# Performance work log

Hardware: AMD Instinct MI355X
Metric: run time of the kernel (lower is better)

Reference implementation:

```python
import jax, jax.numpy as jnp
import numpy as np

N = 50000   # nodes
IN = 256    # in_feats
OUT = 256   # out_feats
R = 4       # num relations
E = 80000   # edges per relation


def setup_inputs() -> dict:
    key = jax.random.key(0)
    ks = jax.random.split(key, 5)
    x = jax.random.normal(ks[0], (N, IN), jnp.float32)
    src = jax.random.randint(ks[1], (R, E), 0, N, jnp.int32)
    dst = jax.random.randint(ks[2], (R, E), 0, N, jnp.int32)
    # xavier_uniform with relu gain sqrt(2)
    limit = np.sqrt(2.0) * np.sqrt(6.0 / (IN + OUT))
    weight = jax.random.uniform(ks[3], (R, IN, OUT), jnp.float32, -limit, limit)
    self_loop_weight = jax.random.uniform(ks[4], (IN, OUT), jnp.float32, -limit, limit)
    bias = jnp.zeros((OUT,), jnp.float32)
    return dict(x=x, src=src, dst=dst, weight=weight,
                self_loop_weight=self_loop_weight, bias=bias)


def reference(x, src, dst, weight, self_loop_weight, bias):
    n = x.shape[0]

    def per_rel(s, d, W):
        # GraphConv(norm='right', weight=W): sum incoming messages, divide by
        # in-degree (clamped to 1), then matmul (in_feats == out_feats path).
        agg = jax.ops.segment_sum(x[s], d, num_segments=n)            # [N, IN]
        deg = jax.ops.segment_sum(jnp.ones(d.shape, x.dtype), d, num_segments=n)
        agg = agg / jnp.maximum(deg, 1.0)[:, None]
        return agg @ W                                                # [N, OUT]

    # HeteroGraphConv default aggregation: sum over relations
    msg = jax.vmap(per_rel)(src, dst, weight).sum(axis=0)             # [N, OUT]
    out = msg + x @ self_loop_weight + bias
    return jax.nn.relu(out)
```

## Files before the change

### kernel.cpp

```cpp
#include <hip/hip_runtime.h>

#define NODES 50000
#define FEAT  256
#define RELS  4
#define EDGES 80000
#define NEDGE (RELS * EDGES)
#define NB    (RELS * NODES)
#define NBSC  196
#define KSTEPS 40
#define CHUNKEL ((size_t)NODES * FEAT)

typedef __bf16 bf16x8  __attribute__((ext_vector_type(8)));
typedef float  floatx4 __attribute__((ext_vector_type(4)));

struct BF8U { union { unsigned short u[8]; bf16x8 v; uint4 q; }; };

static __device__ __forceinline__ unsigned short f2bf(float f) {
  union { float f; unsigned u; } v; v.f = f;
  unsigned r = v.u + 0x7FFFu + ((v.u >> 16) & 1u);
  return (unsigned short)(r >> 16);
}
static __device__ __forceinline__ bf16x8 cvt8(const float* p, float s) {
  float4 a = ((const float4*)p)[0], b = ((const float4*)p)[1];
  BF8U r;
  r.u[0] = f2bf(a.x * s); r.u[1] = f2bf(a.y * s);
  r.u[2] = f2bf(a.z * s); r.u[3] = f2bf(a.w * s);
  r.u[4] = f2bf(b.x * s); r.u[5] = f2bf(b.y * s);
  r.u[6] = f2bf(b.z * s); r.u[7] = f2bf(b.w * s);
  return r.v;
}

__global__ __launch_bounds__(256) void zero_kernel(unsigned* __restrict__ cnt) {
  int i = blockIdx.x * 256 + threadIdx.x;
  if (i < NB) cnt[i] = 0u;
}

__global__ __launch_bounds__(256) void count_kernel(const int* __restrict__ dst,
                                                    unsigned* __restrict__ cnt) {
  int e = blockIdx.x * 256 + threadIdx.x;
  if (e < NEDGE) atomicAdd(&cnt[(e / EDGES) * NODES + dst[e]], 1u);
}

__global__ __launch_bounds__(256) void scan1_kernel(const unsigned* __restrict__ cnt,
                                                    unsigned* __restrict__ bsum) {
  __shared__ unsigned red[4];
  int t = threadIdx.x;
  int i = blockIdx.x * 1024 + t * 4;
  unsigned s = 0;
  if (i + 3 < NB) {
    uint4 v = *(const uint4*)(cnt + i);
    s = v.x + v.y + v.z + v.w;
  } else {
    for (int j = 0; j < 4; ++j) if (i + j < NB) s += cnt[i + j];
  }
  for (int o = 32; o > 0; o >>= 1) s += __shfl_down(s, o);
  if ((t & 63) == 0) red[t >> 6] = s;
  __syncthreads();
  if (t == 0) bsum[blockIdx.x] = red[0] + red[1] + red[2] + red[3];
}

__global__ __launch_bounds__(256) void scan2_kernel(unsigned* __restrict__ bsum) {
  __shared__ unsigned sa[256], sb[256];
  int t = threadIdx.x;
  unsigned v = (t < NBSC) ? bsum[t] : 0u;
  sa[t] = v;
  __syncthreads();
  unsigned* pin = sa; unsigned* pout = sb;
  for (int d = 1; d < 256; d <<= 1) {
    pout[t] = pin[t] + ((t >= d) ? pin[t - d] : 0u);
    __syncthreads();
    unsigned* tmp = pin; pin = pout; pout = tmp;
  }
  if (t < NBSC) bsum[t] = pin[t] - v;
}

__global__ __launch_bounds__(256) void scan3_kernel(const unsigned* __restrict__ cnt,
                                                    const unsigned* __restrict__ bsum,
                                                    unsigned* __restrict__ off,
                                                    unsigned* __restrict__ cur) {
  __shared__ unsigned sa[256], sb[256];
  int t = threadIdx.x;
  int i = blockIdx.x * 1024 + t * 4;
  uint4 v = {0u, 0u, 0u, 0u};
  if (i + 3 < NB) {
    v = *(const uint4*)(cnt + i);
  } else {
    unsigned tmp[4] = {0u, 0u, 0u, 0u};
    for (int j = 0; j < 4; ++j) if (i + j < NB) tmp[j] = cnt[i + j];
    v.x = tmp[0]; v.y = tmp[1]; v.z = tmp[2]; v.w = tmp[3];
  }
  unsigned s = v.x + v.y + v.z + v.w;
  sa[t] = s;
  __syncthreads();
  unsigned* pin = sa; unsigned* pout = sb;
  for (int d = 1; d < 256; d <<= 1) {
    pout[t] = pin[t] + ((t >= d) ? pin[t - d] : 0u);
    __syncthreads();
    unsigned* tmp = pin; pin = pout; pout = tmp;
  }
  unsigned base = bsum[blockIdx.x] + pin[t] - s;
  uint4 o;
  o.x = base; o.y = o.x + v.x; o.z = o.y + v.y; o.w = o.z + v.z;
  if (i + 3 < NB) {
    *(uint4*)(off + i) = o;
    *(uint4*)(cur + i) = o;
  } else {
    unsigned oo[4] = {o.x, o.y, o.z, o.w};
    for (int j = 0; j < 4; ++j) if (i + j < NB) { off[i + j] = oo[j]; cur[i + j] = oo[j]; }
  }
  if (blockIdx.x == 0 && t == 0) off[NB] = NEDGE;
}

__global__ __launch_bounds__(256) void fill_kernel(const int* __restrict__ src,
                                                   const int* __restrict__ dst,
                                                   unsigned* __restrict__ cur,
                                                   unsigned* __restrict__ epk) {
  int e = blockIdx.x * 256 + threadIdx.x;
  if (e < NEDGE) {
    int r = e / EDGES;
    unsigned pos = atomicAdd(&cur[r * NODES + dst[e]], 1u);
    epk[pos] = (unsigned)src[e];
  }
}

__global__ __launch_bounds__(256) void prepack_kernel(const float* __restrict__ w,
                                                      const float* __restrict__ sw,
                                                      unsigned short* __restrict__ bpk) {
  int t = blockIdx.x * 256 + threadIdx.x;
  int ln = t & 63, nc = (t >> 6) & 15, kc = t >> 10;
  int col = nc * 16 + (ln & 15);
  int row0 = kc * 32 + (ln >> 4) * 8;
  BF8U vv;
#pragma unroll
  for (int j = 0; j < 8; ++j) {
    int gk = row0 + j;
    int c = gk >> 8, kr = gk & 255;
    const float* sp = (c < 4) ? (w + (size_t)c * 65536) : sw;
    vv.u[j] = f2bf(sp[(size_t)kr * 256 + col]);
  }
  ((uint4*)bpk)[t] = vv.q;
}

__global__ __launch_bounds__(256) void gather_kernel(
    const float* __restrict__ x, const unsigned* __restrict__ off,
    const unsigned* __restrict__ epk, unsigned short* __restrict__ agg) {
  int b = blockIdx.x * 4 + (threadIdx.x >> 6);
  int lane = threadIdx.x & 63;
  if (b >= NB) return;
  unsigned lo = off[b], hi = off[b + 1];
  float4 acc = {0.f, 0.f, 0.f, 0.f};
  unsigned e = lo;
  for (; e + 2 <= hi; e += 2) {
    int s0 = (int)epk[e], s1 = (int)epk[e + 1];
    float4 v0 = *(const float4*)(x + (size_t)s0 * FEAT + lane * 4);
    float4 v1 = *(const float4*)(x + (size_t)s1 * FEAT + lane * 4);
    acc.x += v0.x + v1.x; acc.y += v0.y + v1.y;
    acc.z += v0.z + v1.z; acc.w += v0.w + v1.w;
  }
  if (e < hi) {
    int s = (int)epk[e];
    float4 v = *(const float4*)(x + (size_t)s * FEAT + lane * 4);
    acc.x += v.x; acc.y += v.y; acc.z += v.z; acc.w += v.w;
  }
  unsigned dg = hi - lo;
  float sc = 1.0f / (float)(dg ? dg : 1u);
  unsigned short o[4] = { f2bf(acc.x * sc), f2bf(acc.y * sc),
                          f2bf(acc.z * sc), f2bf(acc.w * sc) };
  *(uint2*)(agg + (size_t)b * FEAT + lane * 4) = *(const uint2*)o;
}

__global__ __launch_bounds__(256, 3) void gemm_kernel(
    const unsigned short* __restrict__ agg, const float* __restrict__ x,
    const unsigned short* __restrict__ bpk, const float* __restrict__ bias,
    float* __restrict__ out) {
  __shared__ uint4 sA[4][256];
  const int tid = threadIdx.x;
  const int lane = tid & 63, wave = tid >> 6;
  const int quad = lane >> 4, l15 = lane & 15;
  const int m0 = blockIdx.x * 64;
  const int nbase = wave * 4;

  const int sl = tid & 3;
  const int trow = tid >> 2;
  int row_g = m0 + trow; if (row_g >= NODES) row_g = NODES - 1;
  const int widx = trow * 4 + (sl ^ ((trow >> 1) & 3));
  const int pswz = quad ^ ((l15 >> 1) & 3);

  const uint4* aggu4 = (const uint4*)agg;

  auto loadA = [&](int t) -> uint4 {
    if (t < 32) {
      return aggu4[(size_t)(t >> 3) * (CHUNKEL / 8) + (size_t)row_g * 32 +
                   (size_t)((t & 7) * 4 + sl)];
    } else {
      BF8U r;
      r.v = cvt8(x + (size_t)row_g * 256 + (t & 7) * 32 + sl * 8, 1.0f);
      return r.q;
    }
  };

#define SYNC_TILE()                                                            \
  do {                                                                         \
    asm volatile("s_waitcnt lgkmcnt(0)" ::: "memory");                         \
    __builtin_amdgcn_sched_barrier(0);                                         \
    __builtin_amdgcn_s_barrier();                                              \
    __builtin_amdgcn_sched_barrier(0);                                         \
  } while (0)

#define READ_A(bidx, dst)                                                      \
  { _Pragma("unroll") for (int ms = 0; ms < 4; ++ms)                           \
      dst[ms].q = sA[bidx][(ms * 16 + l15) * 4 + pswz]; }

#define LOAD_B(kc, dst)                                                        \
  {                                                                            \
    _Pragma("unroll") for (int ns = 0; ns < 4; ++ns) {                         \
      BF8U t_; t_.q = bp4[(size_t)(kc) * 1024 + (nbase + ns) * 64 + lane];     \
      dst[ns] = t_.v;                                                          \
    }                                                                          \
  }
#define MFMA16(af, bf)                                                         \
  _Pragma("unroll") for (int ms = 0; ms < 4; ++ms)                             \
    _Pragma("unroll") for (int ns = 0; ns < 4; ++ns)                           \
      acc[ms][ns] = __builtin_amdgcn_mfma_f32_16x16x32_bf16(af[ms].v, bf[ns],  \
                                                            acc[ms][ns], 0, 0, 0);

  floatx4 acc[4][4] = {};
  const uint4* bp4 = (const uint4*)bpk;
  bf16x8 b0[4], b1[4];
  BF8U a[4];

  uint4 rP = loadA(0);
  uint4 rO = loadA(1);
  uint4 rE = loadA(2);
  sA[0][widx] = rP;
  LOAD_B(0, b0);
  SYNC_TILE();

  for (int kc = 0; kc < KSTEPS; kc += 2) {
    READ_A(kc & 3, a);
    sA[(kc + 1) & 3][widx] = rO;
    if (kc + 3 < KSTEPS) rO = loadA(kc + 3);
    LOAD_B(kc + 1, b1);
    MFMA16(a, b0);
    SYNC_TILE();

    READ_A((kc + 1) & 3, a);
    if (kc + 2 < KSTEPS) {
      sA[(kc + 2) & 3][widx] = rE;
      LOAD_B(kc + 2, b0);
    }
    if (kc + 4 < KSTEPS) rE = loadA(kc + 4);
    MFMA16(a, b1);
    SYNC_TILE();
  }
#undef SYNC_TILE
#undef READ_A
#undef LOAD_B
#undef MFMA16

#pragma unroll
  for (int ms = 0; ms < 4; ++ms)
#pragma unroll
    for (int i = 0; i < 4; ++i) {
      int row = m0 + ms * 16 + quad * 4 + i;
      if (row < NODES) {
        float* op = out + (size_t)row * FEAT + wave * 64;
#pragma unroll
        for (int ns = 0; ns < 4; ++ns) {
          int col = ns * 16 + l15;
          op[col] = fmaxf(acc[ms][ns][i] + bias[wave * 64 + col], 0.0f);
        }
      }
    }
}

#define AROWS 128
#define ASTR  260
#define ABLK  512

__global__ __launch_bounds__(ABLK) void rgcn_fallback(
    const float* __restrict__ x, const int* __restrict__ src,
    const int* __restrict__ dst, const float* __restrict__ w,
    const float* __restrict__ sw, const float* __restrict__ bias,
    float* __restrict__ out) {
  __shared__ float sAgg[AROWS * ASTR];
  __shared__ unsigned short sB[8192];
  __shared__ unsigned sDeg[AROWS];
  const int tid = threadIdx.x, wave = tid >> 6, lane = tid & 63;
  const int quad = lane >> 4, l15 = lane & 15;
  const int m0 = blockIdx.x * AROWS;
  const int wrow = wave * 16;
  floatx4 acc[16] = {};
  const floatx4 fz = {0.f, 0.f, 0.f, 0.f};
  for (int r = 0; r < RELS; ++r) {
    for (int t = tid; t < (AROWS * ASTR) / 4; t += ABLK) ((floatx4*)sAgg)[t] = fz;
    if (tid < AROWS) sDeg[tid] = 0u;
    __syncthreads();
    const int4* sr4 = (const int4*)(src + r * EDGES);
    const int4* dr4 = (const int4*)(dst + r * EDGES);
    for (int i0 = tid; i0 < 20480; i0 += ABLK) {
      int4 d4 = {-1, -1, -1, -1}, s4 = {0, 0, 0, 0};
      if (i0 < EDGES / 4) { d4 = dr4[i0]; s4 = sr4[i0]; }
      int dd[4] = {d4.x, d4.y, d4.z, d4.w};
      int ss[4] = {s4.x, s4.y, s4.z, s4.w};
#pragma unroll
      for (int j = 0; j < 4; ++j) {
        unsigned u = (unsigned)(dd[j] - m0);
        unsigned long long mb = __ballot(u < (unsigned)AROWS);
        while (mb) {
          int jl = (int)__ffsll(mb) - 1; mb &= mb - 1;
          int s = __shfl(ss[j], jl);
          int ul = __shfl((int)u, jl);
          if (lane == 0) atomicAdd(&sDeg[ul], 1u);
          const float* xp = x + (size_t)s * FEAT + lane;
          float* ap = sAgg + ul * ASTR + lane;
#pragma unroll
          for (int k = 0; k < 4; ++k) atomicAdd(ap + k * 64, xp[k * 64]);
        }
      }
    }
    __syncthreads();
    unsigned dg = sDeg[wrow + l15];
    float rs = 1.0f / (float)(dg ? dg : 1u);
    const float* Wc = w + (size_t)r * 65536;
    for (int kc = 0; kc < 8; ++kc) {
      for (int t = tid; t < 1024; t += ABLK) {
        int ln = t & 63, nc = t >> 6;
        const float* wp = Wc + (size_t)(kc * 32 + (ln >> 4) * 8) * 256 + nc * 16 + (ln & 15);
        BF8U vv;
#pragma unroll
        for (int j = 0; j < 8; ++j) vv.u[j] = f2bf(wp[(size_t)j * 256]);
        ((uint4*)sB)[t] = vv.q;
      }
      __syncthreads();
      bf16x8 a = cvt8(&sAgg[(wrow + l15) * ASTR + kc * 32 + quad * 8], rs);
#pragma unroll
      for (int ns = 0; ns < 16; ++ns) {
        BF8U b8; b8.q = ((const uint4*)sB)[ns * 64 + lane];
        acc[ns] = __builtin_amdgcn_mfma_f32_16x16x32_bf16(a, b8.v, acc[ns], 0, 0, 0);
      }
      __syncthreads();
    }
  }
  {
    int row = m0 + wrow + l15;
    if (row >= NODES) row = NODES - 1;
    for (int kc = 0; kc < 8; ++kc) {
      for (int t = tid; t < 1024; t += ABLK) {
        int ln = t & 63, nc = t >> 6;
        const float* wp = sw + (size_t)(kc * 32 + (ln >> 4) * 8) * 256 + nc * 16 + (ln & 15);
        BF8U vv;
#pragma unroll
        for (int j = 0; j < 8; ++j) vv.u[j] = f2bf(wp[(size_t)j * 256]);
        ((uint4*)sB)[t] = vv.q;
      }
      __syncthreads();
      bf16x8 a = cvt8(x + (size_t)row * FEAT + kc * 32 + quad * 8, 1.0f);
#pragma unroll
      for (int ns = 0; ns < 16; ++ns) {
        BF8U b8; b8.q = ((const uint4*)sB)[ns * 64 + lane];
        acc[ns] = __builtin_amdgcn_mfma_f32_16x16x32_bf16(a, b8.v, acc[ns], 0, 0, 0);
      }
      __syncthreads();
    }
  }
#pragma unroll
  for (int i = 0; i < 4; ++i) {
    int row = m0 + wrow + quad * 4 + i;
    if (row < NODES) {
      float* op = out + (size_t)row * FEAT;
#pragma unroll
      for (int ns = 0; ns < 16; ++ns) {
        int col = ns * 16 + l15;
        op[col] = fmaxf(acc[ns][i] + bias[col], 0.0f);
      }
    }
  }
}

extern "C" void kernel_launch(void* const* d_in, const int* in_sizes, int n_in,
                              void* d_out, int out_size, void* d_ws, size_t ws_size,
                              hipStream_t stream) {
  const float* x    = (const float*)d_in[0];
  const int*   src  = (const int*)d_in[1];
  const int*   dst  = (const int*)d_in[2];
  const float* w    = (const float*)d_in[3];
  const float* sw   = (const float*)d_in[4];
  const float* bias = (const float*)d_in[5];
  float*       out  = (float*)d_out;
  char* ws = (char*)d_ws;

  const size_t NEED = 106736400;
  if (ws_size >= NEED) {
    unsigned short* bpk = (unsigned short*)ws;
    unsigned* cnt  = (unsigned*)(ws + 655360);
    unsigned* off  = (unsigned*)(ws + 1455360);
    unsigned* cur  = (unsigned*)(ws + 2255376);
    unsigned* epk  = (unsigned*)(ws + 3055376);
    unsigned* bsum = (unsigned*)(ws + 4335376);
    unsigned short* agg = (unsigned short*)(ws + 4336400);

    zero_kernel<<<(NB + 255) / 256, 256, 0, stream>>>(cnt);
    count_kernel<<<(NEDGE + 255) / 256, 256, 0, stream>>>(dst, cnt);
    scan1_kernel<<<NBSC, 256, 0, stream>>>(cnt, bsum);
    scan2_kernel<<<1, 256, 0, stream>>>(bsum);
    scan3_kernel<<<NBSC, 256, 0, stream>>>(cnt, bsum, off, cur);
    fill_kernel<<<(NEDGE + 255) / 256, 256, 0, stream>>>(src, dst, cur, epk);
    prepack_kernel<<<160, 256, 0, stream>>>(w, sw, bpk);
    gather_kernel<<<(NB + 3) / 4, 256, 0, stream>>>(x, off, epk, agg);
    gemm_kernel<<<(NODES + 63) / 64, 256, 0, stream>>>(agg, x, bpk, bias, out);
  } else {
    rgcn_fallback<<<391, ABLK, 0, stream>>>(x, src, dst, w, sw, bias, out);
  }
}
```

Before: 259.6 us.

## Fuse CSR build, prepack and gather into one persistent kernel with grid barriers

Replaces eight separate launches (zero, count, three scan stages, fill, prepack, gather) with one persistent kernel of 1536 blocks that separates the phases with atomic-counter grid barriers, plus a memset of the barrier counter. The aim is to remove per-launch overhead and the idle gaps between the small setup kernels. The gather loop is also unrolled to four edges per iteration to put more loads in flight. The grid barrier assumes all 1536 blocks are co-resident (8 per CU is requested via launch bounds), and it risks deadlock or spin overhead if they are not.

```diff
diff --git a/kernel.cpp b/kernel.cpp
--- a/kernel.cpp
+++ b/kernel.cpp
@@ -9,6 +9,8 @@
 #define NBSC  196
 #define KSTEPS 40
 #define CHUNKEL ((size_t)NODES * FEAT)
+#define CBLK  1536
+#define CTHR  (CBLK * 256)
 
 typedef __bf16 bf16x8  __attribute__((ext_vector_type(8)));
 typedef float  floatx4 __attribute__((ext_vector_type(4)));
@@ -30,143 +32,165 @@
   return r.v;
 }
 
-__global__ __launch_bounds__(256) void zero_kernel(unsigned* __restrict__ cnt) {
-  int i = blockIdx.x * 256 + threadIdx.x;
-  if (i < NB) cnt[i] = 0u;
-}
-
-__global__ __launch_bounds__(256) void count_kernel(const int* __restrict__ dst,
-                                                    unsigned* __restrict__ cnt) {
-  int e = blockIdx.x * 256 + threadIdx.x;
-  if (e < NEDGE) atomicAdd(&cnt[(e / EDGES) * NODES + dst[e]], 1u);
-}
-
-__global__ __launch_bounds__(256) void scan1_kernel(const unsigned* __restrict__ cnt,
-                                                    unsigned* __restrict__ bsum) {
+static __device__ __forceinline__ void gbar(unsigned* bar, unsigned tgt) {
+  __syncthreads();
+  if (threadIdx.x == 0) {
+    __hip_atomic_fetch_add(bar, 1u, __ATOMIC_RELEASE, __HIP_MEMORY_SCOPE_AGENT);
+    while (__hip_atomic_load(bar, __ATOMIC_ACQUIRE, __HIP_MEMORY_SCOPE_AGENT) < tgt)
+      __builtin_amdgcn_s_sleep(2);
+  }
+  __syncthreads();
+}
+
+__global__ __launch_bounds__(256, 8) void setup_gather_kernel(
+    const float* __restrict__ x, const int* __restrict__ src,
+    const int* __restrict__ dst, const float* __restrict__ w,
+    const float* __restrict__ sw,
+    unsigned* __restrict__ cnt, unsigned* __restrict__ off,
+    unsigned* __restrict__ cur, unsigned* __restrict__ epk,
+    unsigned* __restrict__ bsum, unsigned* __restrict__ bar,
+    unsigned short* __restrict__ bpk, unsigned short* __restrict__ agg) {
+  __shared__ unsigned sa[256], sb[256];
   __shared__ unsigned red[4];
-  int t = threadIdx.x;
-  int i = blockIdx.x * 1024 + t * 4;
-  unsigned s = 0;
-  if (i + 3 < NB) {
-    uint4 v = *(const uint4*)(cnt + i);
-    s = v.x + v.y + v.z + v.w;
-  } else {
-    for (int j = 0; j < 4; ++j) if (i + j < NB) s += cnt[i + j];
-  }
-  for (int o = 32; o > 0; o >>= 1) s += __shfl_down(s, o);
-  if ((t & 63) == 0) red[t >> 6] = s;
-  __syncthreads();
-  if (t == 0) bsum[blockIdx.x] = red[0] + red[1] + red[2] + red[3];
-}
-
-__global__ __launch_bounds__(256) void scan2_kernel(unsigned* __restrict__ bsum) {
-  __shared__ unsigned sa[256], sb[256];
-  int t = threadIdx.x;
-  unsigned v = (t < NBSC) ? bsum[t] : 0u;
-  sa[t] = v;
-  __syncthreads();
-  unsigned* pin = sa; unsigned* pout = sb;
-  for (int d = 1; d < 256; d <<= 1) {
-    pout[t] = pin[t] + ((t >= d) ? pin[t - d] : 0u);
+  const int tid = threadIdx.x;
+  const int gid = blockIdx.x * 256 + tid;
+
+  for (int i = gid; i < NB; i += CTHR) cnt[i] = 0u;
+  for (int t = gid; t < 40960; t += CTHR) {
+    int ln = t & 63, nc = (t >> 6) & 15, kc = t >> 10;
+    int col = nc * 16 + (ln & 15);
+    int row0 = kc * 32 + (ln >> 4) * 8;
+    BF8U vv;
+#pragma unroll
+    for (int j = 0; j < 8; ++j) {
+      int gk = row0 + j;
+      int c = gk >> 8, kr = gk & 255;
+      const float* sp = (c < 4) ? (w + (size_t)c * 65536) : sw;
+      vv.u[j] = f2bf(sp[(size_t)kr * 256 + col]);
+    }
+    ((uint4*)bpk)[t] = vv.q;
+  }
+  gbar(bar, CBLK * 1);
+
+  for (int e = gid; e < NEDGE; e += CTHR)
+    atomicAdd(&cnt[(e / EDGES) * NODES + dst[e]], 1u);
+  gbar(bar, CBLK * 2);
+
+  {
+    int vb = blockIdx.x;
+    if (vb < NBSC) {
+      int i = vb * 1024 + tid * 4;
+      unsigned s = 0;
+      if (i + 3 < NB) {
+        uint4 v = *(const uint4*)(cnt + i);
+        s = v.x + v.y + v.z + v.w;
+      } else {
+        for (int j = 0; j < 4; ++j) if (i + j < NB) s += cnt[i + j];
+      }
+      for (int o = 32; o > 0; o >>= 1) s += __shfl_down(s, o);
+      if ((tid & 63) == 0) red[tid >> 6] = s;
+      __syncthreads();
+      if (tid == 0) bsum[vb] = red[0] + red[1] + red[2] + red[3];
+    }
+  }
+  gbar(bar, CBLK * 3);
+
+  if (blockIdx.x == 0) {
+    unsigned v = (tid < NBSC) ? bsum[tid] : 0u;
+    sa[tid] = v;
     __syncthreads();
-    unsigned* tmp = pin; pin = pout; pout = tmp;
-  }
-  if (t < NBSC) bsum[t] = pin[t] - v;
-}
-
-__global__ __launch_bounds__(256) void scan3_kernel(const unsigned* __restrict__ cnt,
-                                                    const unsigned* __restrict__ bsum,
-                                                    unsigned* __restrict__ off,
-                                                    unsigned* __restrict__ cur) {
-  __shared__ unsigned sa[256], sb[256];
-  int t = threadIdx.x;
-  int i = blockIdx.x * 1024 + t * 4;
-  uint4 v = {0u, 0u, 0u, 0u};
-  if (i + 3 < NB) {
-    v = *(const uint4*)(cnt + i);
-  } else {
-    unsigned tmp[4] = {0u, 0u, 0u, 0u};
-    for (int j = 0; j < 4; ++j) if (i + j < NB) tmp[j] = cnt[i + j];
-    v.x = tmp[0]; v.y = tmp[1]; v.z = tmp[2]; v.w = tmp[3];
-  }
-  unsigned s = v.x + v.y + v.z + v.w;
-  sa[t] = s;
-  __syncthreads();
-  unsigned* pin = sa; unsigned* pout = sb;
-  for (int d = 1; d < 256; d <<= 1) {
-    pout[t] = pin[t] + ((t >= d) ? pin[t - d] : 0u);
-    __syncthreads();
-    unsigned* tmp = pin; pin = pout; pout = tmp;
-  }
-  unsigned base = bsum[blockIdx.x] + pin[t] - s;
-  uint4 o;
-  o.x = base; o.y = o.x + v.x; o.z = o.y + v.y; o.w = o.z + v.z;
-  if (i + 3 < NB) {
-    *(uint4*)(off + i) = o;
-    *(uint4*)(cur + i) = o;
-  } else {
-    unsigned oo[4] = {o.x, o.y, o.z, o.w};
-    for (int j = 0; j < 4; ++j) if (i + j < NB) { off[i + j] = oo[j]; cur[i + j] = oo[j]; }
-  }
-  if (blockIdx.x == 0 && t == 0) off[NB] = NEDGE;
-}
-
-__global__ __launch_bounds__(256) void fill_kernel(const int* __restrict__ src,
-                                                   const int* __restrict__ dst,
-                                                   unsigned* __restrict__ cur,
-                                                   unsigned* __restrict__ epk) {
-  int e = blockIdx.x * 256 + threadIdx.x;
-  if (e < NEDGE) {
+    unsigned* pin = sa; unsigned* pout = sb;
+    for (int d = 1; d < 256; d <<= 1) {
+      pout[tid] = pin[tid] + ((tid >= d) ? pin[tid - d] : 0u);
+      __syncthreads();
+      unsigned* tmp = pin; pin = pout; pout = tmp;
+    }
+    if (tid < NBSC) bsum[tid] = pin[tid] - v;
+  }
+  gbar(bar, CBLK * 4);
+
+  {
+    int vb = blockIdx.x;
+    if (vb < NBSC) {
+      int i = vb * 1024 + tid * 4;
+      uint4 v = {0u, 0u, 0u, 0u};
+      if (i + 3 < NB) {
+        v = *(const uint4*)(cnt + i);
+      } else {
+        unsigned tmp[4] = {0u, 0u, 0u, 0u};
+        for (int j = 0; j < 4; ++j) if (i + j < NB) tmp[j] = cnt[i + j];
+        v.x = tmp[0]; v.y = tmp[1]; v.z = tmp[2]; v.w = tmp[3];
+      }
+      unsigned s = v.x + v.y + v.z + v.w;
+      sa[tid] = s;
+      __syncthreads();
+      unsigned* pin = sa; unsigned* pout = sb;
+      for (int d = 1; d < 256; d <<= 1) {
+        pout[tid] = pin[tid] + ((tid >= d) ? pin[tid - d] : 0u);
+        __syncthreads();
+        unsigned* tmp = pin; pin = pout; pout = tmp;
+      }
+      unsigned base = bsum[vb] + pin[tid] - s;
+      uint4 o;
+      o.x = base; o.y = o.x + v.x; o.z = o.y + v.y; o.w = o.z + v.z;
+      if (i + 3 < NB) {
+        *(uint4*)(off + i) = o;
+        *(uint4*)(cur + i) = o;
+      } else {
+        unsigned oo[4] = {o.x, o.y, o.z, o.w};
+        for (int j = 0; j < 4; ++j)
+          if (i + j < NB) { off[i + j] = oo[j]; cur[i + j] = oo[j]; }
+      }
+      if (vb == 0 && tid == 0) off[NB] = NEDGE;
+    }
+  }
+  gbar(bar, CBLK * 5);
+
+  for (int e = gid; e < NEDGE; e += CTHR) {
     int r = e / EDGES;
     unsigned pos = atomicAdd(&cur[r * NODES + dst[e]], 1u);
     epk[pos] = (unsigned)src[e];
   }
-}
-
-__global__ __launch_bounds__(256) void prepack_kernel(const float* __restrict__ w,
-                                                      const float* __restrict__ sw,
-                                                      unsigned short* __restrict__ bpk) {
-  int t = blockIdx.x * 256 + threadIdx.x;
-  int ln = t & 63, nc = (t >> 6) & 15, kc = t >> 10;
-  int col = nc * 16 + (ln & 15);
-  int row0 = kc * 32 + (ln >> 4) * 8;
-  BF8U vv;
-#pragma unroll
-  for (int j = 0; j < 8; ++j) {
-    int gk = row0 + j;
-    int c = gk >> 8, kr = gk & 255;
-    const float* sp = (c < 4) ? (w + (size_t)c * 65536) : sw;
-    vv.u[j] = f2bf(sp[(size_t)kr * 256 + col]);
-  }
-  ((uint4*)bpk)[t] = vv.q;
-}
-
-__global__ __launch_bounds__(256) void gather_kernel(
-    const float* __restrict__ x, const unsigned* __restrict__ off,
-    const unsigned* __restrict__ epk, unsigned short* __restrict__ agg) {
-  int b = blockIdx.x * 4 + (threadIdx.x >> 6);
-  int lane = threadIdx.x & 63;
-  if (b >= NB) return;
-  unsigned lo = off[b], hi = off[b + 1];
-  float4 acc = {0.f, 0.f, 0.f, 0.f};
-  unsigned e = lo;
-  for (; e + 2 <= hi; e += 2) {
-    int s0 = (int)epk[e], s1 = (int)epk[e + 1];
-    float4 v0 = *(const float4*)(x + (size_t)s0 * FEAT + lane * 4);
-    float4 v1 = *(const float4*)(x + (size_t)s1 * FEAT + lane * 4);
-    acc.x += v0.x + v1.x; acc.y += v0.y + v1.y;
-    acc.z += v0.z + v1.z; acc.w += v0.w + v1.w;
-  }
-  if (e < hi) {
-    int s = (int)epk[e];
-    float4 v = *(const float4*)(x + (size_t)s * FEAT + lane * 4);
-    acc.x += v.x; acc.y += v.y; acc.z += v.z; acc.w += v.w;
-  }
-  unsigned dg = hi - lo;
-  float sc = 1.0f / (float)(dg ? dg : 1u);
-  unsigned short o[4] = { f2bf(acc.x * sc), f2bf(acc.y * sc),
-                          f2bf(acc.z * sc), f2bf(acc.w * sc) };
-  *(uint2*)(agg + (size_t)b * FEAT + lane * 4) = *(const uint2*)o;
+  gbar(bar, CBLK * 6);
+
+  {
+    const int lane = tid & 63;
+    int wId = blockIdx.x * 4 + (tid >> 6);
+    for (int b = wId; b < NB; b += CBLK * 4) {
+      unsigned lo = off[b], hi = off[b + 1];
+      float4 acc = {0.f, 0.f, 0.f, 0.f};
+      unsigned e = lo;
+      for (; e + 4 <= hi; e += 4) {
+        int s0 = (int)epk[e],     s1 = (int)epk[e + 1];
+        int s2 = (int)epk[e + 2], s3 = (int)epk[e + 3];
+        float4 v0 = *(const float4*)(x + (size_t)s0 * FEAT + lane * 4);
+        float4 v1 = *(const float4*)(x + (size_t)s1 * FEAT + lane * 4);
+        float4 v2 = *(const float4*)(x + (size_t)s2 * FEAT + lane * 4);
+        float4 v3 = *(const float4*)(x + (size_t)s3 * FEAT + lane * 4);
+        acc.x += v0.x + v1.x; acc.y += v0.y + v1.y;
+        acc.z += v0.z + v1.z; acc.w += v0.w + v1.w;
+        acc.x += v2.x + v3.x; acc.y += v2.y + v3.y;
+        acc.z += v2.z + v3.z; acc.w += v2.w + v3.w;
+      }
+      for (; e + 2 <= hi; e += 2) {
+        int s0 = (int)epk[e], s1 = (int)epk[e + 1];
+        float4 v0 = *(const float4*)(x + (size_t)s0 * FEAT + lane * 4);
+        float4 v1 = *(const float4*)(x + (size_t)s1 * FEAT + lane * 4);
+        acc.x += v0.x + v1.x; acc.y += v0.y + v1.y;
+        acc.z += v0.z + v1.z; acc.w += v0.w + v1.w;
+      }
+      if (e < hi) {
+        int s = (int)epk[e];
+        float4 v = *(const float4*)(x + (size_t)s * FEAT + lane * 4);
+        acc.x += v.x; acc.y += v.y; acc.z += v.z; acc.w += v.w;
+      }
+      unsigned dg = hi - lo;
+      float sc = 1.0f / (float)(dg ? dg : 1u);
+      unsigned short o[4] = { f2bf(acc.x * sc), f2bf(acc.y * sc),
+                              f2bf(acc.z * sc), f2bf(acc.w * sc) };
+      *(uint2*)(agg + (size_t)b * FEAT + lane * 4) = *(const uint2*)o;
+    }
+  }
 }
 
 __global__ __launch_bounds__(256, 3) void gemm_kernel(
@@ -398,16 +422,12 @@
     unsigned* cur  = (unsigned*)(ws + 2255376);
     unsigned* epk  = (unsigned*)(ws + 3055376);
     unsigned* bsum = (unsigned*)(ws + 4335376);
+    unsigned* bar  = (unsigned*)(ws + 4336160);
     unsigned short* agg = (unsigned short*)(ws + 4336400);
 
-    zero_kernel<<<(NB + 255) / 256, 256, 0, stream>>>(cnt);
-    count_kernel<<<(NEDGE + 255) / 256, 256, 0, stream>>>(dst, cnt);
-    scan1_kernel<<<NBSC, 256, 0, stream>>>(cnt, bsum);
-    scan2_kernel<<<1, 256, 0, stream>>>(bsum);
-    scan3_kernel<<<NBSC, 256, 0, stream>>>(cnt, bsum, off, cur);
-    fill_kernel<<<(NEDGE + 255) / 256, 256, 0, stream>>>(src, dst, cur, epk);
-    prepack_kernel<<<160, 256, 0, stream>>>(w, sw, bpk);
-    gather_kernel<<<(NB + 3) / 4, 256, 0, stream>>>(x, off, epk, agg);
+    hipMemsetAsync(bar, 0, 64, stream);
+    setup_gather_kernel<<<CBLK, 256, 0, stream>>>(
+        x, src, dst, w, sw, cnt, off, cur, epk, bsum, bar, bpk, agg);
     gemm_kernel<<<(NODES + 63) / 64, 256, 0, stream>>>(agg, x, bpk, bias, out);
   } else {
     rgcn_fallback<<<391, ABLK, 0, stream>>>(x, src, dst, w, sw, bias, out);
```

New measurement: 1.024 ms. 294% more time.

## Fuse setup kernels, use single-pass decoupled-lookback scan, unroll gather by four

Applied to the files above, without the earlier changes.

Weight prepacking is merged into the counter-zeroing kernel, and the three-kernel prefix scan becomes one kernel using a decoupled lookback over per-block status flags. This cuts the launch count from nine to six and removes the serialized single-block scan stage. The gather loop is also unrolled to four edges per iteration so more loads are in flight. The lookback relies on blocks being scheduled in order and adds spin-wait overhead; with only 196 blocks that is likely fine.

```diff
diff --git a/kernel.cpp b/kernel.cpp
--- a/kernel.cpp
+++ b/kernel.cpp
@@ -30,9 +30,28 @@
   return r.v;
 }
 
-__global__ __launch_bounds__(256) void zero_kernel(unsigned* __restrict__ cnt) {
-  int i = blockIdx.x * 256 + threadIdx.x;
-  if (i < NB) cnt[i] = 0u;
+__global__ __launch_bounds__(256) void init_kernel(const float* __restrict__ w,
+                                                   const float* __restrict__ sw,
+                                                   unsigned* __restrict__ cnt,
+                                                   unsigned* __restrict__ state,
+                                                   unsigned short* __restrict__ bpk) {
+  int gid = blockIdx.x * 256 + threadIdx.x;
+  if (gid < NB) cnt[gid] = 0u;
+  if (gid < NBSC) state[gid] = 0u;
+  if (gid < 40960) {
+    int ln = gid & 63, nc = (gid >> 6) & 15, kc = gid >> 10;
+    int col = nc * 16 + (ln & 15);
+    int row0 = kc * 32 + (ln >> 4) * 8;
+    BF8U vv;
+#pragma unroll
+    for (int j = 0; j < 8; ++j) {
+      int gk = row0 + j;
+      int c = gk >> 8, kr = gk & 255;
+      const float* sp = (c < 4) ? (w + (size_t)c * 65536) : sw;
+      vv.u[j] = f2bf(sp[(size_t)kr * 256 + col]);
+    }
+    ((uint4*)bpk)[gid] = vv.q;
+  }
 }
 
 __global__ __launch_bounds__(256) void count_kernel(const int* __restrict__ dst,
@@ -41,46 +60,15 @@
   if (e < NEDGE) atomicAdd(&cnt[(e / EDGES) * NODES + dst[e]], 1u);
 }
 
-__global__ __launch_bounds__(256) void scan1_kernel(const unsigned* __restrict__ cnt,
-                                                    unsigned* __restrict__ bsum) {
-  __shared__ unsigned red[4];
-  int t = threadIdx.x;
-  int i = blockIdx.x * 1024 + t * 4;
-  unsigned s = 0;
-  if (i + 3 < NB) {
-    uint4 v = *(const uint4*)(cnt + i);
-    s = v.x + v.y + v.z + v.w;
-  } else {
-    for (int j = 0; j < 4; ++j) if (i + j < NB) s += cnt[i + j];
-  }
-  for (int o = 32; o > 0; o >>= 1) s += __shfl_down(s, o);
-  if ((t & 63) == 0) red[t >> 6] = s;
-  __syncthreads();
-  if (t == 0) bsum[blockIdx.x] = red[0] + red[1] + red[2] + red[3];
-}
-
-__global__ __launch_bounds__(256) void scan2_kernel(unsigned* __restrict__ bsum) {
+__global__ __launch_bounds__(256) void scan_kernel(const unsigned* __restrict__ cnt,
+                                                   unsigned* __restrict__ state,
+                                                   unsigned* __restrict__ off,
+                                                   unsigned* __restrict__ cur) {
   __shared__ unsigned sa[256], sb[256];
-  int t = threadIdx.x;
-  unsigned v = (t < NBSC) ? bsum[t] : 0u;
-  sa[t] = v;
-  __syncthreads();
-  unsigned* pin = sa; unsigned* pout = sb;
-  for (int d = 1; d < 256; d <<= 1) {
-    pout[t] = pin[t] + ((t >= d) ? pin[t - d] : 0u);
-    __syncthreads();
-    unsigned* tmp = pin; pin = pout; pout = tmp;
-  }
-  if (t < NBSC) bsum[t] = pin[t] - v;
-}
-
-__global__ __launch_bounds__(256) void scan3_kernel(const unsigned* __restrict__ cnt,
-                                                    const unsigned* __restrict__ bsum,
-                                                    unsigned* __restrict__ off,
-                                                    unsigned* __restrict__ cur) {
-  __shared__ unsigned sa[256], sb[256];
-  int t = threadIdx.x;
-  int i = blockIdx.x * 1024 + t * 4;
+  __shared__ unsigned sbase;
+  const int t = threadIdx.x;
+  const int vb = blockIdx.x;
+  const int i = vb * 1024 + t * 4;
   uint4 v = {0u, 0u, 0u, 0u};
   if (i + 3 < NB) {
     v = *(const uint4*)(cnt + i);
@@ -98,7 +86,32 @@
     __syncthreads();
     unsigned* tmp = pin; pin = pout; pout = tmp;
   }
-  unsigned base = bsum[blockIdx.x] + pin[t] - s;
+  if (t == 255) {
+    unsigned total = pin[255];
+    if (vb == 0) {
+      __hip_atomic_store(&state[0], (2u << 30) | total,
+                         __ATOMIC_RELEASE, __HIP_MEMORY_SCOPE_AGENT);
+      sbase = 0u;
+    } else {
+      __hip_atomic_store(&state[vb], (1u << 30) | total,
+                         __ATOMIC_RELEASE, __HIP_MEMORY_SCOPE_AGENT);
+      unsigned run = 0; int j = vb - 1;
+      while (true) {
+        unsigned st = __hip_atomic_load(&state[j],
+                                        __ATOMIC_ACQUIRE, __HIP_MEMORY_SCOPE_AGENT);
+        unsigned fl = st >> 30;
+        if (fl == 0u) { __builtin_amdgcn_s_sleep(1); continue; }
+        run += st & 0x3FFFFFFFu;
+        if (fl == 2u) break;
+        --j;
+      }
+      __hip_atomic_store(&state[vb], (2u << 30) | (run + total),
+                         __ATOMIC_RELEASE, __HIP_MEMORY_SCOPE_AGENT);
+      sbase = run;
+    }
+  }
+  __syncthreads();
+  unsigned base = sbase + pin[t] - s;
   uint4 o;
   o.x = base; o.y = o.x + v.x; o.z = o.y + v.y; o.w = o.z + v.z;
   if (i + 3 < NB) {
@@ -108,7 +121,7 @@
     unsigned oo[4] = {o.x, o.y, o.z, o.w};
     for (int j = 0; j < 4; ++j) if (i + j < NB) { off[i + j] = oo[j]; cur[i + j] = oo[j]; }
   }
-  if (blockIdx.x == 0 && t == 0) off[NB] = NEDGE;
+  if (vb == 0 && t == 0) off[NB] = NEDGE;
 }
 
 __global__ __launch_bounds__(256) void fill_kernel(const int* __restrict__ src,
@@ -123,24 +136,6 @@
   }
 }
 
-__global__ __launch_bounds__(256) void prepack_kernel(const float* __restrict__ w,
-                                                      const float* __restrict__ sw,
-                                                      unsigned short* __restrict__ bpk) {
-  int t = blockIdx.x * 256 + threadIdx.x;
-  int ln = t & 63, nc = (t >> 6) & 15, kc = t >> 10;
-  int col = nc * 16 + (ln & 15);
-  int row0 = kc * 32 + (ln >> 4) * 8;
-  BF8U vv;
-#pragma unroll
-  for (int j = 0; j < 8; ++j) {
-    int gk = row0 + j;
-    int c = gk >> 8, kr = gk & 255;
-    const float* sp = (c < 4) ? (w + (size_t)c * 65536) : sw;
-    vv.u[j] = f2bf(sp[(size_t)kr * 256 + col]);
-  }
-  ((uint4*)bpk)[t] = vv.q;
-}
-
 __global__ __launch_bounds__(256) void gather_kernel(
     const float* __restrict__ x, const unsigned* __restrict__ off,
     const unsigned* __restrict__ epk, unsigned short* __restrict__ agg) {
@@ -150,6 +145,18 @@
   unsigned lo = off[b], hi = off[b + 1];
   float4 acc = {0.f, 0.f, 0.f, 0.f};
   unsigned e = lo;
+  for (; e + 4 <= hi; e += 4) {
+    int s0 = (int)epk[e],     s1 = (int)epk[e + 1];
+    int s2 = (int)epk[e + 2], s3 = (int)epk[e + 3];
+    float4 v0 = *(const float4*)(x + (size_t)s0 * FEAT + lane * 4);
+    float4 v1 = *(const float4*)(x + (size_t)s1 * FEAT + lane * 4);
+    float4 v2 = *(const float4*)(x + (size_t)s2 * FEAT + lane * 4);
+    float4 v3 = *(const float4*)(x + (size_t)s3 * FEAT + lane * 4);
+    acc.x += v0.x + v1.x; acc.y += v0.y + v1.y;
+    acc.z += v0.z + v1.z; acc.w += v0.w + v1.w;
+    acc.x += v2.x + v3.x; acc.y += v2.y + v3.y;
+    acc.z += v2.z + v3.z; acc.w += v2.w + v3.w;
+  }
   for (; e + 2 <= hi; e += 2) {
     int s0 = (int)epk[e], s1 = (int)epk[e + 1];
     float4 v0 = *(const float4*)(x + (size_t)s0 * FEAT + lane * 4);
@@ -393,20 +400,17 @@
   const size_t NEED = 106736400;
   if (ws_size >= NEED) {
     unsigned short* bpk = (unsigned short*)ws;
-    unsigned* cnt  = (unsigned*)(ws + 655360);
-    unsigned* off  = (unsigned*)(ws + 1455360);
-    unsigned* cur  = (unsigned*)(ws + 2255376);
-    unsigned* epk  = (unsigned*)(ws + 3055376);
-    unsigned* bsum = (unsigned*)(ws + 4335376);
+    unsigned* cnt   = (unsigned*)(ws + 655360);
+    unsigned* off   = (unsigned*)(ws + 1455360);
+    unsigned* cur   = (unsigned*)(ws + 2255376);
+    unsigned* epk   = (unsigned*)(ws + 3055376);
+    unsigned* state = (unsigned*)(ws + 4335376);
     unsigned short* agg = (unsigned short*)(ws + 4336400);
 
-    zero_kernel<<<(NB + 255) / 256, 256, 0, stream>>>(cnt);
+    init_kernel<<<(NB + 255) / 256, 256, 0, stream>>>(w, sw, cnt, state, bpk);
     count_kernel<<<(NEDGE + 255) / 256, 256, 0, stream>>>(dst, cnt);
-    scan1_kernel<<<NBSC, 256, 0, stream>>>(cnt, bsum);
-    scan2_kernel<<<1, 256, 0, stream>>>(bsum);
-    scan3_kernel<<<NBSC, 256, 0, stream>>>(cnt, bsum, off, cur);
+    scan_kernel<<<NBSC, 256, 0, stream>>>(cnt, state, off, cur);
     fill_kernel<<<(NEDGE + 255) / 256, 256, 0, stream>>>(src, dst, cur, epk);
-    prepack_kernel<<<160, 256, 0, stream>>>(w, sw, bpk);
     gather_kernel<<<(NB + 3) / 4, 256, 0, stream>>>(x, off, epk, agg);
     gemm_kernel<<<(NODES + 63) / 64, 256, 0, stream>>>(agg, x, bpk, bias, out);
   } else {
```

After: 287.9 us. +10.9%, slower.

## Fuse weight prepack into init kernel and batch four buckets per wave in gather

Applied to the files above, without the earlier changes.

Merges the weight prepack into the counter-zeroing kernel, which removes one launch. Restructures the gather so each wave handles four destination buckets at once. The wave loads the offsets and edge indices cooperatively and broadcasts them with shuffles, then issues up to eight row loads per iteration to raise memory-level parallelism. A serial fallback covers groups with more than 64 edges. The added per-bucket predication adds some divergence and register pressure.

```diff
diff --git a/kernel.cpp b/kernel.cpp
--- a/kernel.cpp
+++ b/kernel.cpp
@@ -30,9 +30,26 @@
   return r.v;
 }
 
-__global__ __launch_bounds__(256) void zero_kernel(unsigned* __restrict__ cnt) {
-  int i = blockIdx.x * 256 + threadIdx.x;
-  if (i < NB) cnt[i] = 0u;
+__global__ __launch_bounds__(256) void init_kernel(const float* __restrict__ w,
+                                                   const float* __restrict__ sw,
+                                                   unsigned* __restrict__ cnt,
+                                                   unsigned short* __restrict__ bpk) {
+  int gid = blockIdx.x * 256 + threadIdx.x;
+  if (gid < NB) cnt[gid] = 0u;
+  if (gid < 40960) {
+    int ln = gid & 63, nc = (gid >> 6) & 15, kc = gid >> 10;
+    int col = nc * 16 + (ln & 15);
+    int row0 = kc * 32 + (ln >> 4) * 8;
+    BF8U vv;
+#pragma unroll
+    for (int j = 0; j < 8; ++j) {
+      int gk = row0 + j;
+      int c = gk >> 8, kr = gk & 255;
+      const float* sp = (c < 4) ? (w + (size_t)c * 65536) : sw;
+      vv.u[j] = f2bf(sp[(size_t)kr * 256 + col]);
+    }
+    ((uint4*)bpk)[gid] = vv.q;
+  }
 }
 
 __global__ __launch_bounds__(256) void count_kernel(const int* __restrict__ dst,
@@ -123,50 +140,90 @@
   }
 }
 
-__global__ __launch_bounds__(256) void prepack_kernel(const float* __restrict__ w,
-                                                      const float* __restrict__ sw,
-                                                      unsigned short* __restrict__ bpk) {
-  int t = blockIdx.x * 256 + threadIdx.x;
-  int ln = t & 63, nc = (t >> 6) & 15, kc = t >> 10;
-  int col = nc * 16 + (ln & 15);
-  int row0 = kc * 32 + (ln >> 4) * 8;
-  BF8U vv;
-#pragma unroll
-  for (int j = 0; j < 8; ++j) {
-    int gk = row0 + j;
-    int c = gk >> 8, kr = gk & 255;
-    const float* sp = (c < 4) ? (w + (size_t)c * 65536) : sw;
-    vv.u[j] = f2bf(sp[(size_t)kr * 256 + col]);
-  }
-  ((uint4*)bpk)[t] = vv.q;
-}
-
 __global__ __launch_bounds__(256) void gather_kernel(
     const float* __restrict__ x, const unsigned* __restrict__ off,
     const unsigned* __restrict__ epk, unsigned short* __restrict__ agg) {
-  int b = blockIdx.x * 4 + (threadIdx.x >> 6);
-  int lane = threadIdx.x & 63;
-  if (b >= NB) return;
-  unsigned lo = off[b], hi = off[b + 1];
-  float4 acc = {0.f, 0.f, 0.f, 0.f};
-  unsigned e = lo;
-  for (; e + 2 <= hi; e += 2) {
-    int s0 = (int)epk[e], s1 = (int)epk[e + 1];
-    float4 v0 = *(const float4*)(x + (size_t)s0 * FEAT + lane * 4);
-    float4 v1 = *(const float4*)(x + (size_t)s1 * FEAT + lane * 4);
-    acc.x += v0.x + v1.x; acc.y += v0.y + v1.y;
-    acc.z += v0.z + v1.z; acc.w += v0.w + v1.w;
-  }
-  if (e < hi) {
-    int s = (int)epk[e];
-    float4 v = *(const float4*)(x + (size_t)s * FEAT + lane * 4);
-    acc.x += v.x; acc.y += v.y; acc.z += v.z; acc.w += v.w;
-  }
-  unsigned dg = hi - lo;
-  float sc = 1.0f / (float)(dg ? dg : 1u);
-  unsigned short o[4] = { f2bf(acc.x * sc), f2bf(acc.y * sc),
-                          f2bf(acc.z * sc), f2bf(acc.w * sc) };
-  *(uint2*)(agg + (size_t)b * FEAT + lane * 4) = *(const uint2*)o;
+  const int lane = threadIdx.x & 63;
+  const int bid = (blockIdx.x * 4 + (threadIdx.x >> 6)) * 4;
+  if (bid >= NB) return;
+
+  unsigned ov = (lane < 5) ? off[bid + lane] : 0u;
+  const unsigned o0 = (unsigned)__shfl((int)ov, 0);
+  const unsigned o1 = (unsigned)__shfl((int)ov, 1);
+  const unsigned o2 = (unsigned)__shfl((int)ov, 2);
+  const unsigned o3 = (unsigned)__shfl((int)ov, 3);
+  const unsigned o4 = (unsigned)__shfl((int)ov, 4);
+  const unsigned lo_w = o0, cnt = o4 - o0;
+
+  const float4 fz = {0.f, 0.f, 0.f, 0.f};
+  float4 A0 = fz, A1 = fz, A2 = fz, A3 = fz;
+
+#define ROW(s) (*(const float4*)(x + (size_t)(s) * FEAT + lane * 4))
+#define STORE(j, A, dcnt)                                                      \
+  {                                                                            \
+    float sc_ = 1.0f / (float)((dcnt) ? (dcnt) : 1u);                          \
+    unsigned short o_[4] = { f2bf((A).x * sc_), f2bf((A).y * sc_),             \
+                             f2bf((A).z * sc_), f2bf((A).w * sc_) };           \
+    *(uint2*)(agg + (size_t)(bid + (j)) * FEAT + lane * 4) =                   \
+        *(const uint2*)o_;                                                     \
+  }
+
+  if (cnt <= 64u) {
+    int ev = ((unsigned)lane < cnt) ? (int)epk[lo_w + (unsigned)lane] : 0;
+    unsigned e0 = o0, e1 = o1, e2 = o2, e3 = o3;
+    const unsigned h0 = o1, h1 = o2, h2 = o3, h3 = o4;
+    while ((e0 < h0) | (e1 < h1) | (e2 < h2) | (e3 < h3)) {
+      const bool q0 = e0 < h0, p0 = e0 + 2 <= h0;
+      const bool q1 = e1 < h1, p1 = e1 + 2 <= h1;
+      const bool q2 = e2 < h2, p2 = e2 + 2 <= h2;
+      const bool q3 = e3 < h3, p3 = e3 + 2 <= h3;
+      float4 u0, w0, u1, w1, u2, w2, u3, w3;
+      if (q0) u0 = ROW(__shfl(ev, (int)(e0 - lo_w)));
+      if (p0) w0 = ROW(__shfl(ev, (int)(e0 + 1u - lo_w)));
+      if (q1) u1 = ROW(__shfl(ev, (int)(e1 - lo_w)));
+      if (p1) w1 = ROW(__shfl(ev, (int)(e1 + 1u - lo_w)));
+      if (q2) u2 = ROW(__shfl(ev, (int)(e2 - lo_w)));
+      if (p2) w2 = ROW(__shfl(ev, (int)(e2 + 1u - lo_w)));
+      if (q3) u3 = ROW(__shfl(ev, (int)(e3 - lo_w)));
+      if (p3) w3 = ROW(__shfl(ev, (int)(e3 + 1u - lo_w)));
+      if (p0) { A0.x += u0.x + w0.x; A0.y += u0.y + w0.y;
+                A0.z += u0.z + w0.z; A0.w += u0.w + w0.w; e0 += 2; }
+      else if (q0) { A0.x += u0.x; A0.y += u0.y; A0.z += u0.z; A0.w += u0.w; ++e0; }
+      if (p1) { A1.x += u1.x + w1.x; A1.y += u1.y + w1.y;
+                A1.z += u1.z + w1.z; A1.w += u1.w + w1.w; e1 += 2; }
+      else if (q1) { A1.x += u1.x; A1.y += u1.y; A1.z += u1.z; A1.w += u1.w; ++e1; }
+      if (p2) { A2.x += u2.x + w2.x; A2.y += u2.y + w2.y;
+                A2.z += u2.z + w2.z; A2.w += u2.w + w2.w; e2 += 2; }
+      else if (q2) { A2.x += u2.x; A2.y += u2.y; A2.z += u2.z; A2.w += u2.w; ++e2; }
+      if (p3) { A3.x += u3.x + w3.x; A3.y += u3.y + w3.y;
+                A3.z += u3.z + w3.z; A3.w += u3.w + w3.w; e3 += 2; }
+      else if (q3) { A3.x += u3.x; A3.y += u3.y; A3.z += u3.z; A3.w += u3.w; ++e3; }
+    }
+    STORE(0, A0, o1 - o0);
+    STORE(1, A1, o2 - o1);
+    STORE(2, A2, o3 - o2);
+    STORE(3, A3, o4 - o3);
+  } else {
+    unsigned losv[5] = {o0, o1, o2, o3, o4};
+    for (int j = 0; j < 4; ++j) {
+      unsigned lo = losv[j], hi = losv[j + 1];
+      float4 acc = fz;
+      unsigned e = lo;
+      for (; e + 2 <= hi; e += 2) {
+        int s0 = (int)epk[e], s1 = (int)epk[e + 1];
+        float4 v0 = ROW(s0), v1 = ROW(s1);
+        acc.x += v0.x + v1.x; acc.y += v0.y + v1.y;
+        acc.z += v0.z + v1.z; acc.w += v0.w + v1.w;
+      }
+      if (e < hi) {
+        float4 v = ROW((int)epk[e]);
+        acc.x += v.x; acc.y += v.y; acc.z += v.z; acc.w += v.w;
+      }
+      STORE(j, acc, hi - lo);
+    }
+  }
+#undef ROW
+#undef STORE
 }
 
 __global__ __launch_bounds__(256, 3) void gemm_kernel(
@@ -400,14 +457,13 @@
     unsigned* bsum = (unsigned*)(ws + 4335376);
     unsigned short* agg = (unsigned short*)(ws + 4336400);
 
-    zero_kernel<<<(NB + 255) / 256, 256, 0, stream>>>(cnt);
+    init_kernel<<<(NB + 255) / 256, 256, 0, stream>>>(w, sw, cnt, bpk);
     count_kernel<<<(NEDGE + 255) / 256, 256, 0, stream>>>(dst, cnt);
     scan1_kernel<<<NBSC, 256, 0, stream>>>(cnt, bsum);
     scan2_kernel<<<1, 256, 0, stream>>>(bsum);
     scan3_kernel<<<NBSC, 256, 0, stream>>>(cnt, bsum, off, cur);
     fill_kernel<<<(NEDGE + 255) / 256, 256, 0, stream>>>(src, dst, cur, epk);
-    prepack_kernel<<<160, 256, 0, stream>>>(w, sw, bpk);
-    gather_kernel<<<(NB + 3) / 4, 256, 0, stream>>>(x, off, epk, agg);
+    gather_kernel<<<NB / 16, 256, 0, stream>>>(x, off, epk, agg);
     gemm_kernel<<<(NODES + 63) / 64, 256, 0, stream>>>(agg, x, bpk, bias, out);
   } else {
     rgcn_fallback<<<391, ABLK, 0, stream>>>(x, src, dst, w, sw, bias, out);
```

New measurement: 255.0 us. About the same (-1.8%).
